# Performance work log

Measured on AMD Instinct MI355X. Metric: run time of the kernel, lower is better.

The kernel has to match this reference:

```python
import jax, jax.numpy as jnp
import numpy as np


def setup_inputs() -> dict:
    key = jax.random.key(0)
    k1, k2 = jax.random.split(key)
    b, c, h, w = 16, 512, 64, 64
    rgb_feat = jax.random.normal(k1, (b, c, h, w), dtype=jnp.float32)
    depth_feat = jax.random.normal(k2, (b, c, h, w), dtype=jnp.float32)
    return {"rgb_feat": rgb_feat, "depth_feat": depth_feat}


def reference(rgb_feat, depth_feat):
    b, c, h, w = rgb_feat.shape
    rgb_r = rgb_feat.reshape(b, c, h * w)      # (b, c, hw)
    depth_r = depth_feat.reshape(b, c, h * w)  # (b, c, hw)
    # interaction: (b, c, c) = depth_r @ rgb_r^T
    interaction = jnp.einsum('bcs,bds->bcd', depth_r, rgb_r)
    interaction = jax.nn.sigmoid(interaction)
    # depth_weighted: (b, c, hw) = interaction @ depth_r
    depth_weighted = jnp.einsum('bcd,bds->bcs', interaction, depth_r)
    fused = rgb_feat + depth_weighted.reshape(b, c, h, w)
    return fused
```

## Files before the change

### kernel.cpp

```cpp
#include <hip/hip_runtime.h>

#define B_ 16
#define C_ 512
#define S_ 4096

typedef __attribute__((ext_vector_type(4))) float float4v;
typedef __attribute__((ext_vector_type(8))) short short8;
typedef __attribute__((ext_vector_type(4))) short short4v;

typedef __attribute__((address_space(1))) unsigned int as1_uint;
typedef __attribute__((address_space(3))) unsigned int as3_uint;

#define ASYNC16(gsrc, ldst) \
  __builtin_amdgcn_global_load_lds((as1_uint*)(gsrc), (as3_uint*)(ldst), 16, 0, 0)

__device__ __forceinline__ unsigned short f2bf(float f) {
  unsigned u = __builtin_bit_cast(unsigned, f);
  u = u + 0x7FFFu + ((u >> 16) & 1u);
  return (unsigned short)(u >> 16);
}

__global__ __launch_bounds__(256) void k_prep(
    const float* __restrict__ depth, const float* __restrict__ rgb,
    unsigned short* __restrict__ depthN, unsigned short* __restrict__ rgbN,
    unsigned short* __restrict__ depthT) {
  __shared__ float tile[64][129];
  int b = blockIdx.z;
  int s0 = blockIdx.x * 64, d0 = blockIdx.y * 128;
  int t = threadIdx.x;
  size_t base = ((size_t)(b * C_ + d0)) * S_ + s0;
  const float* dsrc = depth + base;
  const float* rsrc = rgb + base;
  unsigned short* dN = depthN + base;
  unsigned short* rN = rgbN + base;
#pragma unroll
  for (int it = 0; it < 8; ++it) {
    int slot = it * 256 + t;
    int d = slot >> 4, l16 = slot & 15;
    float4v v = *(const float4v*)(dsrc + d * S_ + l16 * 4);
    tile[l16 * 4 + 0][d] = v.x;
    tile[l16 * 4 + 1][d] = v.y;
    tile[l16 * 4 + 2][d] = v.z;
    tile[l16 * 4 + 3][d] = v.w;
    short4v o = {(short)f2bf(v.x), (short)f2bf(v.y), (short)f2bf(v.z),
                 (short)f2bf(v.w)};
    *(short4v*)(dN + d * S_ + l16 * 4) = o;
    float4v u = *(const float4v*)(rsrc + d * S_ + l16 * 4);
    short4v o2 = {(short)f2bf(u.x), (short)f2bf(u.y), (short)f2bf(u.z),
                  (short)f2bf(u.w)};
    *(short4v*)(rN + d * S_ + l16 * 4) = o2;
  }
  __syncthreads();
  unsigned short* dT = depthT + ((size_t)(b * S_ + s0)) * C_ + d0;
#pragma unroll
  for (int it = 0; it < 8; ++it) {
    int slot = it * 256 + t;
    int s = slot >> 5, l32 = slot & 31;
    float x0 = tile[s][l32 * 4 + 0];
    float x1 = tile[s][l32 * 4 + 1];
    float x2 = tile[s][l32 * 4 + 2];
    float x3 = tile[s][l32 * 4 + 3];
    short4v o = {(short)f2bf(x0), (short)f2bf(x1), (short)f2bf(x2),
                 (short)f2bf(x3)};
    *(short4v*)(dT + s * C_ + l32 * 4) = o;
  }
}

__global__ __launch_bounds__(256) void k_gemm1(
    const unsigned short* __restrict__ depthN,
    const unsigned short* __restrict__ rgbN, unsigned short* __restrict__ I) {
  __shared__ __align__(16) short As[2][64 * 64];
  __shared__ __align__(16) short Bs[2][128 * 64];
  int b = blockIdx.z;
  int c0 = blockIdx.x * 64, d0 = blockIdx.y * 128;
  int t = threadIdx.x;
  const unsigned short* An = depthN + ((size_t)(b * C_ + c0)) * S_;
  const unsigned short* Bn = rgbN + ((size_t)(b * C_ + d0)) * S_;
  int w = t >> 6, l = t & 63, half = l >> 4, r = l & 15;
  int wm = (w >> 1) * 32, wn = (w & 1) * 64;
  float4v acc[2][4] = {};

  auto stage = [&](int bi, int k0) {
#pragma unroll
    for (int q = 0; q < 2; ++q) {
      int idx = q * 256 + t, row = idx >> 3, ch = (idx & 7) ^ (row & 7);
      ASYNC16(An + (size_t)row * S_ + k0 + ch * 8, &As[bi][idx * 8]);
    }
#pragma unroll
    for (int q = 0; q < 4; ++q) {
      int idx = q * 256 + t, row = idx >> 3, ch = (idx & 7) ^ (row & 7);
      ASYNC16(Bn + (size_t)row * S_ + k0 + ch * 8, &Bs[bi][idx * 8]);
    }
  };

  stage(0, 0);
  __syncthreads();
  const int NKT = S_ / 64;
  for (int kt = 0; kt < NKT; ++kt) {
    int cur = kt & 1;
    if (kt + 1 < NKT) stage(cur ^ 1, (kt + 1) * 64);
    short8 af[2][2], bfr[4][2];
#pragma unroll
    for (int i = 0; i < 2; ++i) {
      int row = wm + 16 * i + r;
#pragma unroll
      for (int kk = 0; kk < 2; ++kk)
        af[i][kk] =
            *(const short8*)&As[cur][row * 64 +
                                     (((kk * 4 + half) ^ (row & 7)) * 8)];
    }
#pragma unroll
    for (int j = 0; j < 4; ++j) {
      int row = wn + 16 * j + r;
#pragma unroll
      for (int kk = 0; kk < 2; ++kk)
        bfr[j][kk] =
            *(const short8*)&Bs[cur][row * 64 +
                                     (((kk * 4 + half) ^ (row & 7)) * 8)];
    }
#pragma unroll
    for (int kk = 0; kk < 2; ++kk)
#pragma unroll
      for (int i = 0; i < 2; ++i)
#pragma unroll
        for (int j = 0; j < 4; ++j)
          acc[i][j] = __builtin_amdgcn_mfma_f32_16x16x32_bf16(
              af[i][kk], bfr[j][kk], acc[i][j], 0, 0, 0);
    if (kt + 1 < NKT) __syncthreads();
  }

#pragma unroll
  for (int i = 0; i < 2; ++i)
#pragma unroll
    for (int j = 0; j < 4; ++j)
#pragma unroll
      for (int reg = 0; reg < 4; ++reg) {
        int c = c0 + wm + 16 * i + half * 4 + reg;
        int d = d0 + wn + 16 * j + r;
        float g = 1.0f / (1.0f + __expf(-acc[i][j][reg]));
        I[((size_t)(b * C_ + c)) * C_ + d] = f2bf(g);
      }
}

__global__ __launch_bounds__(256) void k_gemm2(
    const unsigned short* __restrict__ I,
    const unsigned short* __restrict__ depthT, const float* __restrict__ rgb,
    float* __restrict__ out) {
  __shared__ __align__(16) short As[2][128 * 64];
  __shared__ __align__(16) short Bs[2][128 * 64];
  int b = blockIdx.z;
  int c0 = blockIdx.x * 128, s0 = blockIdx.y * 128;
  int t = threadIdx.x;
  const unsigned short* Ab = I + ((size_t)(b * C_ + c0)) * C_;
  const unsigned short* Bb = depthT + ((size_t)(b * S_ + s0)) * C_;
  int w = t >> 6, l = t & 63, half = l >> 4, r = l & 15;
  int wm = (w >> 1) * 64, wn = (w & 1) * 64;
  float4v acc[4][4] = {};

  auto stage = [&](int bi, int k0) {
#pragma unroll
    for (int q = 0; q < 4; ++q) {
      int idx = q * 256 + t, row = idx >> 3, ch = (idx & 7) ^ (row & 7);
      ASYNC16(Ab + (size_t)row * C_ + k0 + ch * 8, &As[bi][idx * 8]);
      ASYNC16(Bb + (size_t)row * C_ + k0 + ch * 8, &Bs[bi][idx * 8]);
    }
  };

  stage(0, 0);
  __syncthreads();
  const int NKT = C_ / 64;
  for (int kt = 0; kt < NKT; ++kt) {
    int cur = kt & 1;
    if (kt + 1 < NKT) stage(cur ^ 1, (kt + 1) * 64);
    short8 af[4][2], bfr[4][2];
#pragma unroll
    for (int i = 0; i < 4; ++i) {
      int rowa = wm + 16 * i + r;
#pragma unroll
      for (int kk = 0; kk < 2; ++kk)
        af[i][kk] =
            *(const short8*)&As[cur][rowa * 64 +
                                     (((kk * 4 + half) ^ (rowa & 7)) * 8)];
      int rowb = wn + 16 * i + r;
#pragma unroll
      for (int kk = 0; kk < 2; ++kk)
        bfr[i][kk] =
            *(const short8*)&Bs[cur][rowb * 64 +
                                     (((kk * 4 + half) ^ (rowb & 7)) * 8)];
    }
#pragma unroll
    for (int kk = 0; kk < 2; ++kk)
#pragma unroll
      for (int i = 0; i < 4; ++i)
#pragma unroll
        for (int j = 0; j < 4; ++j)
          acc[i][j] = __builtin_amdgcn_mfma_f32_16x16x32_bf16(
              af[i][kk], bfr[j][kk], acc[i][j], 0, 0, 0);
    if (kt + 1 < NKT) __syncthreads();
  }

#pragma unroll
  for (int i = 0; i < 4; ++i)
#pragma unroll
    for (int j = 0; j < 4; ++j)
#pragma unroll
      for (int reg = 0; reg < 4; ++reg) {
        int c = c0 + wm + 16 * i + half * 4 + reg;
        int s = s0 + wn + 16 * j + r;
        size_t o = ((size_t)(b * C_ + c)) * S_ + s;
        out[o] = rgb[o] + acc[i][j][reg];
      }
}

extern "C" void kernel_launch(void* const* d_in, const int* in_sizes, int n_in,
                              void* d_out, int out_size, void* d_ws,
                              size_t ws_size, hipStream_t stream) {
  const float* rgb = (const float*)d_in[0];
  const float* depth = (const float*)d_in[1];
  float* out = (float*)d_out;
  unsigned short* depthT = (unsigned short*)d_ws;
  unsigned short* I =
      (unsigned short*)((char*)d_ws + (size_t)B_ * S_ * C_ * 2);
  unsigned short* depthN = (unsigned short*)d_out;
  unsigned short* rgbN = depthN + (size_t)B_ * C_ * S_;

  k_prep<<<dim3(S_ / 64, C_ / 128, B_), 256, 0, stream>>>(depth, rgb, depthN,
                                                          rgbN, depthT);
  k_gemm1<<<dim3(C_ / 64, C_ / 128, B_), 256, 0, stream>>>(depthN, rgbN, I);
  k_gemm2<<<dim3(C_ / 128, S_ / 128, B_), 256, 0, stream>>>(I, depthT, rgb,
                                                            out);
}
```

Baseline: 502.8 us.

## Triple-buffer GEMM pipelines, swizzle block order, and rework prep transpose

Both GEMM kernels move from double to triple buffering. Each uses an explicit vmcnt wait plus barrier so that two tiles of async loads stay in flight, and raises wave priority around the MFMA block. Block indices are remapped with an XCD-style swizzle, and gemm2 drops its K-tile to 32 to fit three stages in LDS. The prep kernel now transposes bf16 values through a smaller XOR-swizzled LDS tile with 16-byte stores. The hand-counted waitcnt values risk ordering errors if the compiler emits extra memory ops, and the smaller K tile halves MFMA work between barriers.

```diff
diff --git a/kernel.cpp b/kernel.cpp
--- a/kernel.cpp
+++ b/kernel.cpp
@@ -13,6 +13,12 @@
 
 #define ASYNC16(gsrc, ldst) \
   __builtin_amdgcn_global_load_lds((as1_uint*)(gsrc), (as3_uint*)(ldst), 16, 0, 0)
+
+#define PIPE_SYNC(N)                                              \
+  do {                                                            \
+    asm volatile("s_waitcnt vmcnt(" #N ")\n\ts_barrier" ::: "memory"); \
+    __builtin_amdgcn_sched_barrier(0);                            \
+  } while (0)
 
 __device__ __forceinline__ unsigned short f2bf(float f) {
   unsigned u = __builtin_bit_cast(unsigned, f);
@@ -24,55 +30,51 @@
     const float* __restrict__ depth, const float* __restrict__ rgb,
     unsigned short* __restrict__ depthN, unsigned short* __restrict__ rgbN,
     unsigned short* __restrict__ depthT) {
-  __shared__ float tile[64][129];
+  __shared__ __align__(16) unsigned short tT[64][72];
   int b = blockIdx.z;
-  int s0 = blockIdx.x * 64, d0 = blockIdx.y * 128;
+  int s0 = blockIdx.x * 64, d0 = blockIdx.y * 64;
   int t = threadIdx.x;
   size_t base = ((size_t)(b * C_ + d0)) * S_ + s0;
-  const float* dsrc = depth + base;
-  const float* rsrc = rgb + base;
-  unsigned short* dN = depthN + base;
-  unsigned short* rN = rgbN + base;
-#pragma unroll
-  for (int it = 0; it < 8; ++it) {
+#pragma unroll
+  for (int it = 0; it < 4; ++it) {
     int slot = it * 256 + t;
     int d = slot >> 4, l16 = slot & 15;
-    float4v v = *(const float4v*)(dsrc + d * S_ + l16 * 4);
-    tile[l16 * 4 + 0][d] = v.x;
-    tile[l16 * 4 + 1][d] = v.y;
-    tile[l16 * 4 + 2][d] = v.z;
-    tile[l16 * 4 + 3][d] = v.w;
-    short4v o = {(short)f2bf(v.x), (short)f2bf(v.y), (short)f2bf(v.z),
-                 (short)f2bf(v.w)};
-    *(short4v*)(dN + d * S_ + l16 * 4) = o;
-    float4v u = *(const float4v*)(rsrc + d * S_ + l16 * 4);
+    size_t off = (size_t)d * S_ + l16 * 4;
+    float4v v = *(const float4v*)(depth + base + off);
+    unsigned short e0 = f2bf(v.x), e1 = f2bf(v.y), e2 = f2bf(v.z),
+                   e3 = f2bf(v.w);
+    short4v o = {(short)e0, (short)e1, (short)e2, (short)e3};
+    *(short4v*)(depthN + base + off) = o;
+    int ss = l16 * 4;
+    tT[ss + 0][(((d >> 3) ^ ((ss + 0) & 7)) << 3) + (d & 7)] = e0;
+    tT[ss + 1][(((d >> 3) ^ ((ss + 1) & 7)) << 3) + (d & 7)] = e1;
+    tT[ss + 2][(((d >> 3) ^ ((ss + 2) & 7)) << 3) + (d & 7)] = e2;
+    tT[ss + 3][(((d >> 3) ^ ((ss + 3) & 7)) << 3) + (d & 7)] = e3;
+    float4v u = *(const float4v*)(rgb + base + off);
     short4v o2 = {(short)f2bf(u.x), (short)f2bf(u.y), (short)f2bf(u.z),
                   (short)f2bf(u.w)};
-    *(short4v*)(rN + d * S_ + l16 * 4) = o2;
+    *(short4v*)(rgbN + base + off) = o2;
   }
   __syncthreads();
   unsigned short* dT = depthT + ((size_t)(b * S_ + s0)) * C_ + d0;
 #pragma unroll
-  for (int it = 0; it < 8; ++it) {
+  for (int it = 0; it < 2; ++it) {
     int slot = it * 256 + t;
-    int s = slot >> 5, l32 = slot & 31;
-    float x0 = tile[s][l32 * 4 + 0];
-    float x1 = tile[s][l32 * 4 + 1];
-    float x2 = tile[s][l32 * 4 + 2];
-    float x3 = tile[s][l32 * 4 + 3];
-    short4v o = {(short)f2bf(x0), (short)f2bf(x1), (short)f2bf(x2),
-                 (short)f2bf(x3)};
-    *(short4v*)(dT + s * C_ + l32 * 4) = o;
+    int s = slot >> 3, g = slot & 7;
+    short8 vv = *(const short8*)&tT[s][(g ^ (s & 7)) << 3];
+    *(short8*)(dT + (size_t)s * C_ + g * 8) = vv;
   }
 }
 
 __global__ __launch_bounds__(256) void k_gemm1(
     const unsigned short* __restrict__ depthN,
     const unsigned short* __restrict__ rgbN, unsigned short* __restrict__ I) {
-  __shared__ __align__(16) short As[2][64 * 64];
-  __shared__ __align__(16) short Bs[2][128 * 64];
-  int b = blockIdx.z;
-  int c0 = blockIdx.x * 64, d0 = blockIdx.y * 128;
+  __shared__ __align__(16) short As[3][64 * 64];
+  __shared__ __align__(16) short Bs[3][128 * 64];
+  int lid = blockIdx.x + 8 * (blockIdx.y + 4 * blockIdx.z);
+  int swz = (lid & 7) * 64 + (lid >> 3);
+  int bx = swz & 7, by = (swz >> 3) & 3, b = swz >> 5;
+  int c0 = bx * 64, d0 = by * 128;
   int t = threadIdx.x;
   const unsigned short* An = depthN + ((size_t)(b * C_ + c0)) * S_;
   const unsigned short* Bn = rgbN + ((size_t)(b * C_ + d0)) * S_;
@@ -94,30 +96,31 @@
   };
 
   stage(0, 0);
-  __syncthreads();
+  stage(1, 64);
+  stage(2, 128);
+  PIPE_SYNC(12);
+
   const int NKT = S_ / 64;
   for (int kt = 0; kt < NKT; ++kt) {
-    int cur = kt & 1;
-    if (kt + 1 < NKT) stage(cur ^ 1, (kt + 1) * 64);
+    int cur = kt % 3;
     short8 af[2][2], bfr[4][2];
 #pragma unroll
     for (int i = 0; i < 2; ++i) {
       int row = wm + 16 * i + r;
 #pragma unroll
       for (int kk = 0; kk < 2; ++kk)
-        af[i][kk] =
-            *(const short8*)&As[cur][row * 64 +
-                                     (((kk * 4 + half) ^ (row & 7)) * 8)];
+        af[i][kk] = *(const short8*)&As[cur][row * 64 +
+                                            (((kk * 4 + half) ^ (row & 7)) * 8)];
     }
 #pragma unroll
     for (int j = 0; j < 4; ++j) {
       int row = wn + 16 * j + r;
 #pragma unroll
       for (int kk = 0; kk < 2; ++kk)
-        bfr[j][kk] =
-            *(const short8*)&Bs[cur][row * 64 +
-                                     (((kk * 4 + half) ^ (row & 7)) * 8)];
-    }
+        bfr[j][kk] = *(const short8*)&Bs[cur][row * 64 +
+                                             (((kk * 4 + half) ^ (row & 7)) * 8)];
+    }
+    __builtin_amdgcn_s_setprio(1);
 #pragma unroll
     for (int kk = 0; kk < 2; ++kk)
 #pragma unroll
@@ -126,7 +129,13 @@
         for (int j = 0; j < 4; ++j)
           acc[i][j] = __builtin_amdgcn_mfma_f32_16x16x32_bf16(
               af[i][kk], bfr[j][kk], acc[i][j], 0, 0, 0);
-    if (kt + 1 < NKT) __syncthreads();
+    __builtin_amdgcn_s_setprio(0);
+    if (kt + 2 < NKT) {
+      PIPE_SYNC(6);
+    } else if (kt + 1 < NKT) {
+      PIPE_SYNC(0);
+    }
+    if (kt + 3 < NKT) stage(cur, (kt + 3) * 64);
   }
 
 #pragma unroll
@@ -146,10 +155,12 @@
     const unsigned short* __restrict__ I,
     const unsigned short* __restrict__ depthT, const float* __restrict__ rgb,
     float* __restrict__ out) {
-  __shared__ __align__(16) short As[2][128 * 64];
-  __shared__ __align__(16) short Bs[2][128 * 64];
-  int b = blockIdx.z;
-  int c0 = blockIdx.x * 128, s0 = blockIdx.y * 128;
+  __shared__ __align__(16) short As[3][128 * 32];
+  __shared__ __align__(16) short Bs[3][128 * 32];
+  int lid = blockIdx.x + 4 * (blockIdx.y + 32 * blockIdx.z);
+  int swz = (lid & 7) * 256 + (lid >> 3);
+  int bx = swz & 3, by = (swz >> 2) & 31, b = swz >> 7;
+  int c0 = bx * 128, s0 = by * 128;
   int t = threadIdx.x;
   const unsigned short* Ab = I + ((size_t)(b * C_ + c0)) * C_;
   const unsigned short* Bb = depthT + ((size_t)(b * S_ + s0)) * C_;
@@ -159,44 +170,45 @@
 
   auto stage = [&](int bi, int k0) {
 #pragma unroll
-    for (int q = 0; q < 4; ++q) {
-      int idx = q * 256 + t, row = idx >> 3, ch = (idx & 7) ^ (row & 7);
+    for (int q = 0; q < 2; ++q) {
+      int idx = q * 256 + t, row = idx >> 2, ch = (idx & 3) ^ (row & 3);
       ASYNC16(Ab + (size_t)row * C_ + k0 + ch * 8, &As[bi][idx * 8]);
       ASYNC16(Bb + (size_t)row * C_ + k0 + ch * 8, &Bs[bi][idx * 8]);
     }
   };
 
   stage(0, 0);
-  __syncthreads();
-  const int NKT = C_ / 64;
+  stage(1, 32);
+  stage(2, 64);
+  PIPE_SYNC(8);
+
+  const int NKT = C_ / 32;
   for (int kt = 0; kt < NKT; ++kt) {
-    int cur = kt & 1;
-    if (kt + 1 < NKT) stage(cur ^ 1, (kt + 1) * 64);
-    short8 af[4][2], bfr[4][2];
+    int cur = kt % 3;
+    short8 af[4], bfr[4];
 #pragma unroll
     for (int i = 0; i < 4; ++i) {
       int rowa = wm + 16 * i + r;
-#pragma unroll
-      for (int kk = 0; kk < 2; ++kk)
-        af[i][kk] =
-            *(const short8*)&As[cur][rowa * 64 +
-                                     (((kk * 4 + half) ^ (rowa & 7)) * 8)];
+      af[i] = *(const short8*)&As[cur][rowa * 32 +
+                                       (((half ^ (rowa & 3)) & 3) * 8)];
       int rowb = wn + 16 * i + r;
-#pragma unroll
-      for (int kk = 0; kk < 2; ++kk)
-        bfr[i][kk] =
-            *(const short8*)&Bs[cur][rowb * 64 +
-                                     (((kk * 4 + half) ^ (rowb & 7)) * 8)];
-    }
-#pragma unroll
-    for (int kk = 0; kk < 2; ++kk)
-#pragma unroll
-      for (int i = 0; i < 4; ++i)
-#pragma unroll
-        for (int j = 0; j < 4; ++j)
-          acc[i][j] = __builtin_amdgcn_mfma_f32_16x16x32_bf16(
-              af[i][kk], bfr[j][kk], acc[i][j], 0, 0, 0);
-    if (kt + 1 < NKT) __syncthreads();
+      bfr[i] = *(const short8*)&Bs[cur][rowb * 32 +
+                                        (((half ^ (rowb & 3)) & 3) * 8)];
+    }
+    __builtin_amdgcn_s_setprio(1);
+#pragma unroll
+    for (int i = 0; i < 4; ++i)
+#pragma unroll
+      for (int j = 0; j < 4; ++j)
+        acc[i][j] = __builtin_amdgcn_mfma_f32_16x16x32_bf16(af[i], bfr[j],
+                                                            acc[i][j], 0, 0, 0);
+    __builtin_amdgcn_s_setprio(0);
+    if (kt + 2 < NKT) {
+      PIPE_SYNC(4);
+    } else if (kt + 1 < NKT) {
+      PIPE_SYNC(0);
+    }
+    if (kt + 3 < NKT) stage(cur, (kt + 3) * 32);
   }
 
 #pragma unroll
@@ -224,8 +236,8 @@
   unsigned short* depthN = (unsigned short*)d_out;
   unsigned short* rgbN = depthN + (size_t)B_ * C_ * S_;
 
-  k_prep<<<dim3(S_ / 64, C_ / 128, B_), 256, 0, stream>>>(depth, rgb, depthN,
-                                                          rgbN, depthT);
+  k_prep<<<dim3(S_ / 64, C_ / 64, B_), 256, 0, stream>>>(depth, rgb, depthN,
+                                                         rgbN, depthT);
   k_gemm1<<<dim3(C_ / 64, C_ / 128, B_), 256, 0, stream>>>(depthN, rgbN, I);
   k_gemm2<<<dim3(C_ / 128, S_ / 128, B_), 256, 0, stream>>>(I, depthT, rgb,
                                                             out);
```

Result: no change. 499.4 us (-0.7%).
